# Kernel tuning notes

Hardware: AMD Instinct MI355X
Metric: run time of the kernel (lower is better)

## Reference

```python
import jax, jax.numpy as jnp
import numpy as np

N_NODES = 100000
N_EDGES = 3200000
N_GRAPHS = 64
NEG_SLOPE = 0.2


def mish(x):
    return x * jnp.tanh(jax.nn.softplus(x))


def gat_layer(x, src, dst, W, b, a_src, a_dst, heads, out_ch, n_nodes):
    # h: [N, H, C]
    h = (x @ W).reshape(n_nodes, heads, out_ch)
    alpha_s = jnp.sum(h * a_src[None], axis=-1)  # [N, H]
    alpha_d = jnp.sum(h * a_dst[None], axis=-1)  # [N, H]
    e = jax.nn.leaky_relu(alpha_s[src] + alpha_d[dst], NEG_SLOPE)  # [E, H]
    # scatter-softmax over incoming edges of each destination node
    emax = jax.ops.segment_max(e, dst, num_segments=n_nodes)  # [N, H]
    ee = jnp.exp(e - emax[dst])
    den = jax.ops.segment_sum(ee, dst, num_segments=n_nodes)
    alpha = ee / (den[dst] + 1e-16)  # [E, H]
    msg = h[src] * alpha[..., None]  # [E, H, C]
    out = jax.ops.segment_sum(msg, dst, num_segments=n_nodes)
    return out.reshape(n_nodes, heads * out_ch) + b


def setup_inputs() -> dict:
    key = jax.random.key(0)
    ks = jax.random.split(key, 10)
    x = jax.random.normal(ks[0], (N_NODES, 128), dtype=jnp.float32)
    edge_index = jax.random.randint(ks[1], (2, N_EDGES), 0, N_NODES, dtype=jnp.int64)
    batch = jnp.sort(jax.random.randint(ks[2], (N_NODES,), 0, N_GRAPHS, dtype=jnp.int64))
    s1 = 1.0 / np.sqrt(128.0)
    s2 = 1.0 / np.sqrt(16.0)
    return {
        "x": x,
        "edge_index": edge_index,
        "batch": batch,
        "W1": jax.random.normal(ks[3], (128, 16), dtype=jnp.float32) * s1,
        "b1": jnp.zeros((16,), dtype=jnp.float32),
        "a_src1": jax.random.normal(ks[4], (4, 4), dtype=jnp.float32) * 0.5,
        "a_dst1": jax.random.normal(ks[5], (4, 4), dtype=jnp.float32) * 0.5,
        "W2": jax.random.normal(ks[6], (16, 32), dtype=jnp.float32) * s2,
        "b2": jnp.zeros((32,), dtype=jnp.float32),
        "a_src2": jax.random.normal(ks[7], (1, 32), dtype=jnp.float32) * 0.5,
        "a_dst2": jax.random.normal(ks[8], (1, 32), dtype=jnp.float32) * 0.5,
    }


def reference(x, edge_index, batch, W1, b1, a_src1, a_dst1, W2, b2, a_src2, a_dst2):
    n = x.shape[0]
    # PyG GATConv default add_self_loops=True
    loop = jnp.arange(n, dtype=edge_index.dtype)
    src = jnp.concatenate([edge_index[0], loop])
    dst = jnp.concatenate([edge_index[1], loop])
    h = mish(gat_layer(x, src, dst, W1, b1, a_src1, a_dst1, heads=4, out_ch=4, n_nodes=n))
    h = mish(gat_layer(h, src, dst, W2, b2, a_src2, a_dst2, heads=1, out_ch=32, n_nodes=n))
    # global_mean_pool
    sums = jax.ops.segment_sum(h, batch, num_segments=N_GRAPHS)
    cnts = jax.ops.segment_sum(jnp.ones((n,), h.dtype), batch, num_segments=N_GRAPHS)
    return sums / jnp.maximum(cnts, 1.0)[:, None]
```

## Files before the change

kernel.cpp:

```cpp
#include <hip/hip_runtime.h>
#include <hip/hip_fp16.h>
#include <math.h>

#define NEG_SLOPE 0.2f
#define GB 192
#define SB 320
#define CHMAX 11264
#define CAP 5120
#define CAPH 2560

typedef _Float16 half2v __attribute__((ext_vector_type(2)));
typedef _Float16 half4v __attribute__((ext_vector_type(4)));

__device__ __forceinline__ float mishf(float x) {
    if (x > 15.f) return x;
    float ex = __expf(x);
    float y = 1.f + ex;
    float y2 = y * y;
    return x * (y2 - 1.f) / (y2 + 1.f);
}

__device__ __forceinline__ float lw(float e) {
    return __expf(fmaxf(e, NEG_SLOPE * e));
}

__device__ __forceinline__ float hdot2a(half2v a, half2v b, float c) {
#if __has_builtin(__builtin_amdgcn_fdot2)
    return __builtin_amdgcn_fdot2(a, b, c, false);
#else
    return (float)a.x * (float)b.x + (float)a.y * (float)b.y + c;
#endif
}

__global__ __launch_bounds__(1024) void front_kernel(
        const float* __restrict__ x, const float* __restrict__ W1,
        const float* __restrict__ a_dst,
        const float* __restrict__ W2, const float* __restrict__ as2,
        const float* __restrict__ ad2,
        _Float16* __restrict__ hpre1h, float* __restrict__ addst,
        float* __restrict__ vs, float* __restrict__ vd,
        const int* __restrict__ src, const int* __restrict__ dst,
        int E, int Etot, int CH, int NB, int N, int NT,
        int* __restrict__ cursor, int* __restrict__ pairs) {
    __shared__ __attribute__((aligned(16))) char smem[63824];
    int tid = threadIdx.x;
    if (blockIdx.x < GB) {
        float* Wlt = (float*)smem;
        float* xs  = Wlt + 16 * 132;
        if (blockIdx.x == 0 && tid < 16) {
            float ps = 0.f, pd = 0.f;
            #pragma unroll
            for (int c = 0; c < 32; c++) {
                float w = W2[tid * 32 + c];
                ps += w * as2[c];
                pd += w * ad2[c];
            }
            vs[tid] = ps; vd[tid] = pd;
        }
        for (int i = tid; i < 2048; i += 1024) Wlt[(i & 15) * 132 + (i >> 4)] = W1[i];
        int nl = tid >> 4, ch = tid & 15;
        for (int t = blockIdx.x; t < NT; t += GB) {
            int nodebase = t * 64;
            int nvalid = min(64, N - nodebase);
            __syncthreads();
            const float4* x4 = (const float4*)(x + (size_t)nodebase * 128);
            #pragma unroll
            for (int u = 0; u < 2; u++) {
                int i = tid + (u << 10);
                int tnl = i >> 5;
                if (tnl < nvalid) {
                    float4 v = x4[i];
                    int k = (i & 31) * 4;
                    float* dp = &xs[tnl * 132 + k];
                    dp[0] = v.x; dp[1] = v.y; dp[2] = v.z; dp[3] = v.w;
                }
            }
            __syncthreads();
            if (nl < nvalid) {
                const float4* xr4 = (const float4*)&xs[nl * 132];
                const float4* wr4 = (const float4*)&Wlt[ch * 132];
                float acc = 0.f;
                #pragma unroll
                for (int k4 = 0; k4 < 32; k4++) {
                    float4 xv = xr4[k4];
                    float4 wv = wr4[k4];
                    acc += xv.x * wv.x + xv.y * wv.y + xv.z * wv.z + xv.w * wv.w;
                }
                int node = nodebase + nl;
                hpre1h[node * 16 + ch] = (_Float16)acc;
                float pd = acc * a_dst[ch];
                pd += __shfl_xor(pd, 1); pd += __shfl_xor(pd, 2);
                if ((ch & 3) == 0) addst[node * 4 + (ch >> 2)] = pd;
            }
        }
    } else {
        int nb2 = 2 * NB;
        int* A    = (int*)smem;
        int* Boff = A + nb2;
        int* C    = Boff + nb2;
        int* buf  = C + nb2;
        int blk = blockIdx.x - GB;
        for (int b = tid; b < nb2; b += 1024) A[b] = 0;
        __syncthreads();
        int ibeg = blk * CH, iend = min((blk + 1) * CH, Etot);
        int cdv[11], cs[11];
        #pragma unroll
        for (int u = 0; u < 11; u++) {
            int i = ibeg + tid + (u << 10);
            int d = -1, s = 0;
            if (i < iend) {
                if (i < E) { d = dst[i]; s = src[i]; } else { d = i - E; s = d; }
                atomicAdd(&A[d >> 6], 1);
            }
            cdv[u] = d; cs[u] = s;
        }
        for (int i = ibeg + CHMAX + tid; i < iend; i += 1024) {
            int d, s;
            if (i < E) { d = dst[i]; s = src[i]; } else { d = i - E; s = d; }
            int f = d >> 6;
            int pos = atomicAdd(&cursor[f], 1);
            pos = pos < CAPH ? pos : CAPH - 1;
            size_t addr = (size_t)(f >> 1) * CAP + ((f & 1) ? (CAP - 1 - pos) : pos);
            pairs[addr] = s | ((d & 63) << 17);
        }
        __syncthreads();
        for (int b = tid; b < nb2; b += 1024) Boff[b] = A[b];
        __syncthreads();
        for (int o = 1; o < nb2; o <<= 1) {
            int i1 = tid, i2 = tid + 1024;
            int v1 = 0, v2 = 0;
            if (i1 < nb2 && i1 >= o) v1 = Boff[i1 - o];
            if (i2 < nb2 && i2 >= o) v2 = Boff[i2 - o];
            __syncthreads();
            if (i1 < nb2) Boff[i1] += v1;
            if (i2 < nb2) Boff[i2] += v2;
            __syncthreads();
        }
        for (int b = tid; b < nb2; b += 1024) {
            int cnt = A[b];
            Boff[b] -= cnt;
            C[b] = cnt ? atomicAdd(&cursor[b], cnt) : 0;
        }
        __syncthreads();
        for (int b = tid; b < nb2; b += 1024) A[b] = 0;
        __syncthreads();
        #pragma unroll
        for (int u = 0; u < 11; u++) {
            int d = cdv[u];
            if (d < 0) continue;
            int f = d >> 6;
            int r = atomicAdd(&A[f], 1);
            buf[Boff[f] + r] = cs[u] | ((d & 63) << 17);
        }
        __syncthreads();
        int total = iend - ibeg;
        if (total > CHMAX) total = CHMAX;
        if (total < 0) total = 0;
        for (int j = tid; j < total; j += 1024) {
            int lo = 0, hi = nb2 - 1;
            while (lo < hi) {
                int mid = (lo + hi + 1) >> 1;
                if (Boff[mid] <= j) lo = mid; else hi = mid - 1;
            }
            int f = lo;
            int pos = C[f] + (j - Boff[f]);
            pos = pos < CAPH ? pos : CAPH - 1;
            size_t addr = (size_t)(f >> 1) * CAP + ((f & 1) ? (CAP - 1 - pos) : pos);
            pairs[addr] = buf[j];
        }
    }
}

__global__ __launch_bounds__(256) void csragg1_kernel(
        const int* __restrict__ pairs, const int* __restrict__ btotal,
        int NB, int N,
        int* __restrict__ ssorted, int* __restrict__ rs, int* __restrict__ re,
        const float* __restrict__ a_src1, const float* __restrict__ addst,
        const _Float16* __restrict__ hpre1h, const float* __restrict__ b1,
        const float* __restrict__ vs, const float* __restrict__ vd,
        _Float16* __restrict__ hpost1h,
        float* __restrict__ as2n, float* __restrict__ ad2n) {
    __shared__ int deg[64];
    __shared__ int s[64];
    __shared__ int cur[64];
    __shared__ __attribute__((aligned(16))) int lds_sorted[CAPH];
    int tid = threadIdx.x, bh = blockIdx.x;
    int B = bh >> 1, half = bh & 1;
    int nb0 = (B << 7) + (half << 6);
    int cnt_nodes = min(64, N - nb0);
    int c = min(btotal[bh], CAPH);
    int rbase = B * CAP + (half ? CAP - c : 0);
    if (tid < 64) deg[tid] = 0;
    __syncthreads();
    for (int j = tid; j < c; j += 256)
        atomicAdd(&deg[(pairs[rbase + j] >> 17) & 63], 1);
    __syncthreads();
    if (tid < 64) s[tid] = deg[tid];
    __syncthreads();
    for (int o = 1; o < 64; o <<= 1) {
        int v = 0;
        if (tid < 64 && tid >= o) v = s[tid - o];
        __syncthreads();
        if (tid < 64) s[tid] += v;
        __syncthreads();
    }
    if (tid < 64) {
        int ex = s[tid] - deg[tid];
        cur[tid] = ex;
        if (tid < cnt_nodes) {
            rs[nb0 + tid] = bh * CAPH + ex;
            re[nb0 + tid] = bh * CAPH + ex + deg[tid];
        }
    }
    __syncthreads();
    for (int j = tid; j < c; j += 256) {
        int p = pairs[rbase + j];
        int pos = atomicAdd(&cur[(p >> 17) & 63], 1);
        lds_sorted[pos < CAPH ? pos : CAPH - 1] = p & 0x1FFFF;
    }
    __syncthreads();

    {
        int t4 = c >> 2;
        const int4* ls4 = (const int4*)lds_sorted;
        int4* gs4 = (int4*)(ssorted + (size_t)bh * CAPH);
        for (int j = tid; j < t4; j += 256) gs4[j] = ls4[j];
        for (int j = (t4 << 2) + tid; j < c; j += 256)
            ssorted[(size_t)bh * CAPH + j] = lds_sorted[j];
    }

    int wave = tid >> 6;
    int lane = tid & 63;
    int head = lane & 3, er = lane >> 2;
    int c0 = head * 4;
    half2v w01, w23;
    w01.x = (_Float16)a_src1[c0];     w01.y = (_Float16)a_src1[c0 + 1];
    w23.x = (_Float16)a_src1[c0 + 2]; w23.y = (_Float16)a_src1[c0 + 3];
    for (int r = 0; r < 16; r++) {
        int ln = (wave << 4) + r;
        if (ln >= cnt_nodes) break;
        int node = nb0 + ln;
        int end = cur[ln];
        int start = end - deg[ln];
        float adh = addst[node * 4 + head];
        float den = 0.f, a0 = 0.f, a1 = 0.f, a2 = 0.f, a3 = 0.f;
        int last = end - 1;
        int jb = start;
        for (; jb + 16 <= end; jb += 16) {
            int s0 = lds_sorted[jb + er];
            half4v h = *(const half4v*)(hpre1h + (size_t)s0 * 16 + c0);
            half2v hlo = __builtin_shufflevector(h, h, 0, 1);
            half2v hhi = __builtin_shufflevector(h, h, 2, 3);
            float p = hdot2a(hlo, w01, hdot2a(hhi, w23, 0.f));
            float w = lw(p + adh);
            den += w;
            a0 += (float)h.x * w; a1 += (float)h.y * w;
            a2 += (float)h.z * w; a3 += (float)h.w * w;
        }
        if (jb < end) {
            int j0 = jb + er;
            int k0 = (j0 <= last) ? j0 : last;
            int s0 = lds_sorted[k0];
            half4v h = *(const half4v*)(hpre1h + (size_t)s0 * 16 + c0);
            half2v hlo = __builtin_shufflevector(h, h, 0, 1);
            half2v hhi = __builtin_shufflevector(h, h, 2, 3);
            float p = hdot2a(hlo, w01, hdot2a(hhi, w23, 0.f));
            float w = (j0 <= last) ? lw(p + adh) : 0.f;
            den += w;
            a0 += (float)h.x * w; a1 += (float)h.y * w;
            a2 += (float)h.z * w; a3 += (float)h.w * w;
        }
        a0 += __shfl_xor(a0, 4);  a1 += __shfl_xor(a1, 4);  a2 += __shfl_xor(a2, 4);  a3 += __shfl_xor(a3, 4);  den += __shfl_xor(den, 4);
        a0 += __shfl_xor(a0, 8);  a1 += __shfl_xor(a1, 8);  a2 += __shfl_xor(a2, 8);  a3 += __shfl_xor(a3, 8);  den += __shfl_xor(den, 8);
        a0 += __shfl_xor(a0, 16); a1 += __shfl_xor(a1, 16); a2 += __shfl_xor(a2, 16); a3 += __shfl_xor(a3, 16); den += __shfl_xor(den, 16);
        a0 += __shfl_xor(a0, 32); a1 += __shfl_xor(a1, 32); a2 += __shfl_xor(a2, 32); a3 += __shfl_xor(a3, 32); den += __shfl_xor(den, 32);
        if (er == 0) {
            float inv = 1.f / (den + 1e-16f);
            float o0 = mishf(a0 * inv + b1[c0]);
            float o1 = mishf(a1 * inv + b1[c0 + 1]);
            float o2 = mishf(a2 * inv + b1[c0 + 2]);
            float o3 = mishf(a3 * inv + b1[c0 + 3]);
            half4v oh;
            oh.x = (_Float16)o0; oh.y = (_Float16)o1;
            oh.z = (_Float16)o2; oh.w = (_Float16)o3;
            *(half4v*)(hpost1h + (size_t)node * 16 + c0) = oh;
            float ps = o0 * vs[c0] + o1 * vs[c0 + 1] + o2 * vs[c0 + 2] + o3 * vs[c0 + 3];
            float pd = o0 * vd[c0] + o1 * vd[c0 + 1] + o2 * vd[c0 + 2] + o3 * vd[c0 + 3];
            ps += __shfl_xor(ps, 1); pd += __shfl_xor(pd, 1);
            ps += __shfl_xor(ps, 2); pd += __shfl_xor(pd, 2);
            if (head == 0) { as2n[node] = ps; ad2n[node] = pd; }
        }
    }
}

__global__ void agg2_kernel(const int* __restrict__ rs, const int* __restrict__ re,
                            const int* __restrict__ ssorted,
                            const float* __restrict__ as2n, const float* __restrict__ ad2n,
                            const _Float16* __restrict__ hpost1h,
                            float* __restrict__ agg16, float* __restrict__ denv, int N) {
    int wave = threadIdx.x >> 6;
    int lane = threadIdx.x & 63;
    int node = blockIdx.x * 4 + wave;
    if (node >= N) return;
    int start = rs[node], end = re[node];
    int q = lane & 3, er = lane >> 2;
    int c0 = q * 4;
    float adh = ad2n[node];
    const _Float16* hb = hpost1h + c0;
    float den = 0.f, a0 = 0.f, a1 = 0.f, a2 = 0.f, a3 = 0.f;
    int last = end - 1;
    int jb = start;
    for (; jb + 16 <= end; jb += 16) {
        int s0 = __builtin_nontemporal_load(ssorted + jb + er);
        float w = lw(as2n[s0] + adh);
        half4v h = *(const half4v*)(hb + (size_t)s0 * 16);
        den += w;
        a0 += (float)h.x * w; a1 += (float)h.y * w;
        a2 += (float)h.z * w; a3 += (float)h.w * w;
    }
    if (jb < end) {
        int j0 = jb + er;
        int k0 = (j0 <= last) ? j0 : last;
        int s0 = __builtin_nontemporal_load(ssorted + k0);
        float w = (j0 <= last) ? lw(as2n[s0] + adh) : 0.f;
        half4v h = *(const half4v*)(hb + (size_t)s0 * 16);
        den += w;
        a0 += (float)h.x * w; a1 += (float)h.y * w;
        a2 += (float)h.z * w; a3 += (float)h.w * w;
    }
    a0 += __shfl_xor(a0, 4);  a1 += __shfl_xor(a1, 4);  a2 += __shfl_xor(a2, 4);  a3 += __shfl_xor(a3, 4);  den += __shfl_xor(den, 4);
    a0 += __shfl_xor(a0, 8);  a1 += __shfl_xor(a1, 8);  a2 += __shfl_xor(a2, 8);  a3 += __shfl_xor(a3, 8);  den += __shfl_xor(den, 8);
    a0 += __shfl_xor(a0, 16); a1 += __shfl_xor(a1, 16); a2 += __shfl_xor(a2, 16); a3 += __shfl_xor(a3, 16); den += __shfl_xor(den, 16);
    a0 += __shfl_xor(a0, 32); a1 += __shfl_xor(a1, 32); a2 += __shfl_xor(a2, 32); a3 += __shfl_xor(a3, 32); den += __shfl_xor(den, 32);
    if (er == 0) {
        float4 o; o.x = a0; o.y = a1; o.z = a2; o.w = a3;
        *(float4*)(agg16 + (size_t)node * 16 + c0) = o;
        if (q == 0) denv[node] = den;
    }
}

__global__ void post2pool_kernel(const float* __restrict__ agg16, const float* __restrict__ denv,
                                 const float* __restrict__ W2, const float* __restrict__ b2,
                                 const int* __restrict__ batch,
                                 float* __restrict__ pool, float* __restrict__ cnt, int N) {
    __shared__ float Wl[16 * 32];
    int tid = threadIdx.x;
    for (int i = tid; i < 512; i += 256) Wl[i] = W2[i];
    __syncthreads();
    int r = tid >> 5, ch = tid & 31;
    float bc = b2[ch];
    int base = blockIdx.x * 128;
    int cur = -1;
    float sum = 0.f, c = 0.f;
    for (int it = 0; it < 16; it++) {
        int n = base + it * 8 + r;
        if (n >= N) break;
        int g = batch[n];
        if (g != cur) {
            if (cur >= 0) {
                atomicAdd(&pool[cur * 32 + ch], sum);
                if (ch == 0) atomicAdd(&cnt[cur], c);
            }
            cur = g; sum = 0.f; c = 0.f;
        }
        const float* ar = agg16 + (size_t)n * 16;
        float acc = 0.f;
        #pragma unroll
        for (int k = 0; k < 16; k++) acc += ar[k] * Wl[k * 32 + ch];
        float val = mishf(acc / (denv[n] + 1e-16f) + bc);
        sum += val;
        c += 1.f;
    }
    if (cur >= 0) {
        atomicAdd(&pool[cur * 32 + ch], sum);
        if (ch == 0) atomicAdd(&cnt[cur], c);
    }
}

__global__ void fin_kernel(const float* __restrict__ pool, const float* __restrict__ cnt,
                           float* __restrict__ out, int NG) {
    int i = blockIdx.x * blockDim.x + threadIdx.x;
    if (i >= NG * 32) return;
    out[i] = pool[i] / fmaxf(cnt[i >> 5], 1.0f);
}

extern "C" void kernel_launch(void* const* d_in, const int* in_sizes, int n_in,
                              void* d_out, int out_size, void* d_ws, size_t ws_size,
                              hipStream_t stream) {
    const float* x   = (const float*)d_in[0];
    const int* eidx  = (const int*)d_in[1];
    const int* batch = (const int*)d_in[2];
    const float* W1  = (const float*)d_in[3];
    const float* b1  = (const float*)d_in[4];
    const float* as1 = (const float*)d_in[5];
    const float* ad1 = (const float*)d_in[6];
    const float* W2  = (const float*)d_in[7];
    const float* b2  = (const float*)d_in[8];
    const float* as2 = (const float*)d_in[9];
    const float* ad2 = (const float*)d_in[10];
    float* out = (float*)d_out;

    int N = in_sizes[0] / 128;
    int E = in_sizes[1] / 2;
    int Etot = E + N;
    int NG = out_size / 32;
    const int* esrc = eidx;
    const int* edst = eidx + E;

    int NB = (N + 127) >> 7;
    int NBH = NB * 2;
    int NT = (N + 63) >> 6;
    int CH = (Etot + SB - 1) / SB;

    char* p = (char*)d_ws;
    auto alloc = [&](size_t nbytes) {
        p = (char*)(((uintptr_t)p + 15) & ~(uintptr_t)15);
        void* r = (void*)p; p += nbytes; return r;
    };
    int* pairs        = (int*)alloc((size_t)NB * CAP * 4);
    int* ssorted      = (int*)alloc((size_t)NBH * CAPH * 4);
    int* rs           = (int*)alloc((size_t)N * 4);
    int* re           = (int*)alloc((size_t)N * 4);
    int* cursor       = (int*)alloc((size_t)NBH * 4);
    _Float16* hpre1h  = (_Float16*)alloc((size_t)N * 16 * 2);
    _Float16* hpost1h = (_Float16*)alloc((size_t)N * 16 * 2);
    float* addst1  = (float*)alloc((size_t)N * 4 * 4);
    float* as2n    = (float*)alloc((size_t)N * 4);
    float* ad2n    = (float*)alloc((size_t)N * 4);
    float* agg16   = (float*)alloc((size_t)N * 16 * 4);
    float* denv    = (float*)alloc((size_t)N * 4);
    float* vs      = (float*)alloc(16 * 4);
    float* vd      = (float*)alloc(16 * 4);
    float* pool    = (float*)alloc((size_t)NG * 32 * 4);
    float* cnt     = (float*)alloc((size_t)NG * 4);

    hipMemsetAsync(cursor, 0, (size_t)NBH * 4, stream);
    hipMemsetAsync(pool, 0, (size_t)NG * 32 * 4, stream);
    hipMemsetAsync(cnt, 0, (size_t)NG * 4, stream);

    front_kernel<<<GB + SB, 1024, 0, stream>>>(x, W1, ad1, W2, as2, ad2,
                                               hpre1h, addst1, vs, vd,
                                               esrc, edst, E, Etot, CH, NB, N, NT,
                                               cursor, pairs);
    csragg1_kernel<<<NBH, 256, 0, stream>>>(pairs, cursor, NB, N,
                                            ssorted, rs, re, as1, addst1, hpre1h,
                                            b1, vs, vd, hpost1h, as2n, ad2n);
    agg2_kernel<<<(N + 3) / 4, 256, 0, stream>>>(rs, re, ssorted, as2n, ad2n, hpost1h,
                                                 agg16, denv, N);
    post2pool_kernel<<<(N + 127) / 128, 256, 0, stream>>>(agg16, denv, W2, b2, batch,
                                                          pool, cnt, N);
    fin_kernel<<<(NG * 32 + 255) / 256, 256, 0, stream>>>(pool, cnt, out, NG);
}
```

Measured before the change: 332.9 us.

## Widen per-lane gathers to 16B half8 and double csragg1 block size

The layer-1 and layer-2 aggregation loops now have each lane load 8 halves (16 bytes) per edge instead of 4, with two lanes covering a node's 16 channels. Each lane also handles two edges per iteration, so a wave covers 64 edges at a time and fewer lanes sit in the xor-shuffle reduction. csragg1 moves from 256 to 512 threads per block, so each wave owns 8 nodes instead of 16. This is meant to cut gather instructions and raise memory-level parallelism, at the cost of more wasted lanes on low-degree tails and higher register pressure.

```diff
diff --git a/kernel.cpp b/kernel.cpp
--- a/kernel.cpp
+++ b/kernel.cpp
@@ -11,6 +11,7 @@
 
 typedef _Float16 half2v __attribute__((ext_vector_type(2)));
 typedef _Float16 half4v __attribute__((ext_vector_type(4)));
+typedef _Float16 half8v __attribute__((ext_vector_type(8)));
 
 __device__ __forceinline__ float mishf(float x) {
     if (x > 15.f) return x;
@@ -171,7 +172,7 @@
     }
 }
 
-__global__ __launch_bounds__(256) void csragg1_kernel(
+__global__ __launch_bounds__(512) void csragg1_kernel(
         const int* __restrict__ pairs, const int* __restrict__ btotal,
         int NB, int N,
         int* __restrict__ ssorted, int* __restrict__ rs, int* __restrict__ re,
@@ -192,7 +193,7 @@
     int rbase = B * CAP + (half ? CAP - c : 0);
     if (tid < 64) deg[tid] = 0;
     __syncthreads();
-    for (int j = tid; j < c; j += 256)
+    for (int j = tid; j < c; j += 512)
         atomicAdd(&deg[(pairs[rbase + j] >> 17) & 63], 1);
     __syncthreads();
     if (tid < 64) s[tid] = deg[tid];
@@ -213,7 +214,7 @@
         }
     }
     __syncthreads();
-    for (int j = tid; j < c; j += 256) {
+    for (int j = tid; j < c; j += 512) {
         int p = pairs[rbase + j];
         int pos = atomicAdd(&cur[(p >> 17) & 63], 1);
         lds_sorted[pos < CAPH ? pos : CAPH - 1] = p & 0x1FFFF;
@@ -224,117 +225,170 @@
         int t4 = c >> 2;
         const int4* ls4 = (const int4*)lds_sorted;
         int4* gs4 = (int4*)(ssorted + (size_t)bh * CAPH);
-        for (int j = tid; j < t4; j += 256) gs4[j] = ls4[j];
-        for (int j = (t4 << 2) + tid; j < c; j += 256)
+        for (int j = tid; j < t4; j += 512) gs4[j] = ls4[j];
+        for (int j = (t4 << 2) + tid; j < c; j += 512)
             ssorted[(size_t)bh * CAPH + j] = lds_sorted[j];
     }
 
     int wave = tid >> 6;
     int lane = tid & 63;
-    int head = lane & 3, er = lane >> 2;
-    int c0 = head * 4;
-    half2v w01, w23;
-    w01.x = (_Float16)a_src1[c0];     w01.y = (_Float16)a_src1[c0 + 1];
-    w23.x = (_Float16)a_src1[c0 + 2]; w23.y = (_Float16)a_src1[c0 + 3];
-    for (int r = 0; r < 16; r++) {
-        int ln = (wave << 4) + r;
+    int q = lane & 1, er = lane >> 1;
+    int c0 = q * 8;
+    half2v wA0, wA1, wB0, wB1;
+    wA0.x = (_Float16)a_src1[c0];     wA0.y = (_Float16)a_src1[c0 + 1];
+    wA1.x = (_Float16)a_src1[c0 + 2]; wA1.y = (_Float16)a_src1[c0 + 3];
+    wB0.x = (_Float16)a_src1[c0 + 4]; wB0.y = (_Float16)a_src1[c0 + 5];
+    wB1.x = (_Float16)a_src1[c0 + 6]; wB1.y = (_Float16)a_src1[c0 + 7];
+    for (int r = 0; r < 8; r++) {
+        int ln = (wave << 3) + r;
         if (ln >= cnt_nodes) break;
         int node = nb0 + ln;
         int end = cur[ln];
         int start = end - deg[ln];
-        float adh = addst[node * 4 + head];
-        float den = 0.f, a0 = 0.f, a1 = 0.f, a2 = 0.f, a3 = 0.f;
+        float adh0 = addst[node * 4 + q * 2];
+        float adh1 = addst[node * 4 + q * 2 + 1];
+        float a[8] = {0.f, 0.f, 0.f, 0.f, 0.f, 0.f, 0.f, 0.f};
+        float den0 = 0.f, den1 = 0.f;
         int last = end - 1;
         int jb = start;
-        for (; jb + 16 <= end; jb += 16) {
+        for (; jb + 64 <= end; jb += 64) {
             int s0 = lds_sorted[jb + er];
-            half4v h = *(const half4v*)(hpre1h + (size_t)s0 * 16 + c0);
-            half2v hlo = __builtin_shufflevector(h, h, 0, 1);
-            half2v hhi = __builtin_shufflevector(h, h, 2, 3);
-            float p = hdot2a(hlo, w01, hdot2a(hhi, w23, 0.f));
-            float w = lw(p + adh);
-            den += w;
-            a0 += (float)h.x * w; a1 += (float)h.y * w;
-            a2 += (float)h.z * w; a3 += (float)h.w * w;
+            int s1 = lds_sorted[jb + 32 + er];
+            half8v h0 = *(const half8v*)(hpre1h + (size_t)s0 * 16 + c0);
+            half8v h1 = *(const half8v*)(hpre1h + (size_t)s1 * 16 + c0);
+            half2v h0a = __builtin_shufflevector(h0, h0, 0, 1);
+            half2v h0b = __builtin_shufflevector(h0, h0, 2, 3);
+            half2v h0c = __builtin_shufflevector(h0, h0, 4, 5);
+            half2v h0d = __builtin_shufflevector(h0, h0, 6, 7);
+            half2v h1a = __builtin_shufflevector(h1, h1, 0, 1);
+            half2v h1b = __builtin_shufflevector(h1, h1, 2, 3);
+            half2v h1c = __builtin_shufflevector(h1, h1, 4, 5);
+            half2v h1d = __builtin_shufflevector(h1, h1, 6, 7);
+            float wt00 = lw(hdot2a(h0a, wA0, hdot2a(h0b, wA1, 0.f)) + adh0);
+            float wt01 = lw(hdot2a(h0c, wB0, hdot2a(h0d, wB1, 0.f)) + adh1);
+            float wt10 = lw(hdot2a(h1a, wA0, hdot2a(h1b, wA1, 0.f)) + adh0);
+            float wt11 = lw(hdot2a(h1c, wB0, hdot2a(h1d, wB1, 0.f)) + adh1);
+            den0 += wt00 + wt10; den1 += wt01 + wt11;
+            #pragma unroll
+            for (int k = 0; k < 4; k++) a[k]     += (float)h0[k]     * wt00 + (float)h1[k]     * wt10;
+            #pragma unroll
+            for (int k = 0; k < 4; k++) a[4 + k] += (float)h0[4 + k] * wt01 + (float)h1[4 + k] * wt11;
         }
         if (jb < end) {
-            int j0 = jb + er;
+            int j0 = jb + er, j1 = jb + 32 + er;
             int k0 = (j0 <= last) ? j0 : last;
+            int k1 = (j1 <= last) ? j1 : last;
             int s0 = lds_sorted[k0];
-            half4v h = *(const half4v*)(hpre1h + (size_t)s0 * 16 + c0);
-            half2v hlo = __builtin_shufflevector(h, h, 0, 1);
-            half2v hhi = __builtin_shufflevector(h, h, 2, 3);
-            float p = hdot2a(hlo, w01, hdot2a(hhi, w23, 0.f));
-            float w = (j0 <= last) ? lw(p + adh) : 0.f;
-            den += w;
-            a0 += (float)h.x * w; a1 += (float)h.y * w;
-            a2 += (float)h.z * w; a3 += (float)h.w * w;
-        }
-        a0 += __shfl_xor(a0, 4);  a1 += __shfl_xor(a1, 4);  a2 += __shfl_xor(a2, 4);  a3 += __shfl_xor(a3, 4);  den += __shfl_xor(den, 4);
-        a0 += __shfl_xor(a0, 8);  a1 += __shfl_xor(a1, 8);  a2 += __shfl_xor(a2, 8);  a3 += __shfl_xor(a3, 8);  den += __shfl_xor(den, 8);
-        a0 += __shfl_xor(a0, 16); a1 += __shfl_xor(a1, 16); a2 += __shfl_xor(a2, 16); a3 += __shfl_xor(a3, 16); den += __shfl_xor(den, 16);
-        a0 += __shfl_xor(a0, 32); a1 += __shfl_xor(a1, 32); a2 += __shfl_xor(a2, 32); a3 += __shfl_xor(a3, 32); den += __shfl_xor(den, 32);
+            int s1 = lds_sorted[k1];
+            half8v h0 = *(const half8v*)(hpre1h + (size_t)s0 * 16 + c0);
+            half8v h1 = *(const half8v*)(hpre1h + (size_t)s1 * 16 + c0);
+            half2v h0a = __builtin_shufflevector(h0, h0, 0, 1);
+            half2v h0b = __builtin_shufflevector(h0, h0, 2, 3);
+            half2v h0c = __builtin_shufflevector(h0, h0, 4, 5);
+            half2v h0d = __builtin_shufflevector(h0, h0, 6, 7);
+            half2v h1a = __builtin_shufflevector(h1, h1, 0, 1);
+            half2v h1b = __builtin_shufflevector(h1, h1, 2, 3);
+            half2v h1c = __builtin_shufflevector(h1, h1, 4, 5);
+            half2v h1d = __builtin_shufflevector(h1, h1, 6, 7);
+            float e00 = hdot2a(h0a, wA0, hdot2a(h0b, wA1, 0.f)) + adh0;
+            float e01 = hdot2a(h0c, wB0, hdot2a(h0d, wB1, 0.f)) + adh1;
+            float e10 = hdot2a(h1a, wA0, hdot2a(h1b, wA1, 0.f)) + adh0;
+            float e11 = hdot2a(h1c, wB0, hdot2a(h1d, wB1, 0.f)) + adh1;
+            float wt00 = (j0 <= last) ? lw(e00) : 0.f;
+            float wt01 = (j0 <= last) ? lw(e01) : 0.f;
+            float wt10 = (j1 <= last) ? lw(e10) : 0.f;
+            float wt11 = (j1 <= last) ? lw(e11) : 0.f;
+            den0 += wt00 + wt10; den1 += wt01 + wt11;
+            #pragma unroll
+            for (int k = 0; k < 4; k++) a[k]     += (float)h0[k]     * wt00 + (float)h1[k]     * wt10;
+            #pragma unroll
+            for (int k = 0; k < 4; k++) a[4 + k] += (float)h0[4 + k] * wt01 + (float)h1[4 + k] * wt11;
+        }
+        #pragma unroll
+        for (int off = 2; off <= 32; off <<= 1) {
+            #pragma unroll
+            for (int k = 0; k < 8; k++) a[k] += __shfl_xor(a[k], off);
+            den0 += __shfl_xor(den0, off);
+            den1 += __shfl_xor(den1, off);
+        }
         if (er == 0) {
-            float inv = 1.f / (den + 1e-16f);
-            float o0 = mishf(a0 * inv + b1[c0]);
-            float o1 = mishf(a1 * inv + b1[c0 + 1]);
-            float o2 = mishf(a2 * inv + b1[c0 + 2]);
-            float o3 = mishf(a3 * inv + b1[c0 + 3]);
-            half4v oh;
-            oh.x = (_Float16)o0; oh.y = (_Float16)o1;
-            oh.z = (_Float16)o2; oh.w = (_Float16)o3;
-            *(half4v*)(hpost1h + (size_t)node * 16 + c0) = oh;
-            float ps = o0 * vs[c0] + o1 * vs[c0 + 1] + o2 * vs[c0 + 2] + o3 * vs[c0 + 3];
-            float pd = o0 * vd[c0] + o1 * vd[c0 + 1] + o2 * vd[c0 + 2] + o3 * vd[c0 + 3];
+            float inv0 = 1.f / (den0 + 1e-16f);
+            float inv1 = 1.f / (den1 + 1e-16f);
+            float o[8];
+            #pragma unroll
+            for (int k = 0; k < 4; k++) o[k]     = mishf(a[k]     * inv0 + b1[c0 + k]);
+            #pragma unroll
+            for (int k = 0; k < 4; k++) o[4 + k] = mishf(a[4 + k] * inv1 + b1[c0 + 4 + k]);
+            half8v oh;
+            #pragma unroll
+            for (int k = 0; k < 8; k++) oh[k] = (_Float16)o[k];
+            *(half8v*)(hpost1h + (size_t)node * 16 + c0) = oh;
+            float ps = 0.f, pd = 0.f;
+            #pragma unroll
+            for (int k = 0; k < 8; k++) { ps += o[k] * vs[c0 + k]; pd += o[k] * vd[c0 + k]; }
             ps += __shfl_xor(ps, 1); pd += __shfl_xor(pd, 1);
-            ps += __shfl_xor(ps, 2); pd += __shfl_xor(pd, 2);
-            if (head == 0) { as2n[node] = ps; ad2n[node] = pd; }
-        }
-    }
-}
-
-__global__ void agg2_kernel(const int* __restrict__ rs, const int* __restrict__ re,
-                            const int* __restrict__ ssorted,
-                            const float* __restrict__ as2n, const float* __restrict__ ad2n,
-                            const _Float16* __restrict__ hpost1h,
-                            float* __restrict__ agg16, float* __restrict__ denv, int N) {
+            if (q == 0) { as2n[node] = ps; ad2n[node] = pd; }
+        }
+    }
+}
+
+__global__ __launch_bounds__(256) void agg2_kernel(
+        const int* __restrict__ rs, const int* __restrict__ re,
+        const int* __restrict__ ssorted,
+        const float* __restrict__ as2n, const float* __restrict__ ad2n,
+        const _Float16* __restrict__ hpost1h,
+        float* __restrict__ agg16, float* __restrict__ denv, int N) {
     int wave = threadIdx.x >> 6;
     int lane = threadIdx.x & 63;
     int node = blockIdx.x * 4 + wave;
     if (node >= N) return;
     int start = rs[node], end = re[node];
-    int q = lane & 3, er = lane >> 2;
-    int c0 = q * 4;
+    int q = lane & 1, er = lane >> 1;
+    int c0 = q * 8;
     float adh = ad2n[node];
     const _Float16* hb = hpost1h + c0;
-    float den = 0.f, a0 = 0.f, a1 = 0.f, a2 = 0.f, a3 = 0.f;
+    float a[8] = {0.f, 0.f, 0.f, 0.f, 0.f, 0.f, 0.f, 0.f};
+    float den = 0.f;
     int last = end - 1;
     int jb = start;
-    for (; jb + 16 <= end; jb += 16) {
+    for (; jb + 64 <= end; jb += 64) {
         int s0 = __builtin_nontemporal_load(ssorted + jb + er);
-        float w = lw(as2n[s0] + adh);
-        half4v h = *(const half4v*)(hb + (size_t)s0 * 16);
-        den += w;
-        a0 += (float)h.x * w; a1 += (float)h.y * w;
-        a2 += (float)h.z * w; a3 += (float)h.w * w;
+        int s1 = __builtin_nontemporal_load(ssorted + jb + 32 + er);
+        float wt0 = lw(as2n[s0] + adh);
+        float wt1 = lw(as2n[s1] + adh);
+        half8v h0 = *(const half8v*)(hb + (size_t)s0 * 16);
+        half8v h1 = *(const half8v*)(hb + (size_t)s1 * 16);
+        den += wt0 + wt1;
+        #pragma unroll
+        for (int k = 0; k < 8; k++) a[k] += (float)h0[k] * wt0 + (float)h1[k] * wt1;
     }
     if (jb < end) {
-        int j0 = jb + er;
+        int j0 = jb + er, j1 = jb + 32 + er;
         int k0 = (j0 <= last) ? j0 : last;
+        int k1 = (j1 <= last) ? j1 : last;
         int s0 = __builtin_nontemporal_load(ssorted + k0);
-        float w = (j0 <= last) ? lw(as2n[s0] + adh) : 0.f;
-        half4v h = *(const half4v*)(hb + (size_t)s0 * 16);
-        den += w;
-        a0 += (float)h.x * w; a1 += (float)h.y * w;
-        a2 += (float)h.z * w; a3 += (float)h.w * w;
-    }
-    a0 += __shfl_xor(a0, 4);  a1 += __shfl_xor(a1, 4);  a2 += __shfl_xor(a2, 4);  a3 += __shfl_xor(a3, 4);  den += __shfl_xor(den, 4);
-    a0 += __shfl_xor(a0, 8);  a1 += __shfl_xor(a1, 8);  a2 += __shfl_xor(a2, 8);  a3 += __shfl_xor(a3, 8);  den += __shfl_xor(den, 8);
-    a0 += __shfl_xor(a0, 16); a1 += __shfl_xor(a1, 16); a2 += __shfl_xor(a2, 16); a3 += __shfl_xor(a3, 16); den += __shfl_xor(den, 16);
-    a0 += __shfl_xor(a0, 32); a1 += __shfl_xor(a1, 32); a2 += __shfl_xor(a2, 32); a3 += __shfl_xor(a3, 32); den += __shfl_xor(den, 32);
+        int s1 = __builtin_nontemporal_load(ssorted + k1);
+        float wt0 = (j0 <= last) ? lw(as2n[s0] + adh) : 0.f;
+        float wt1 = (j1 <= last) ? lw(as2n[s1] + adh) : 0.f;
+        half8v h0 = *(const half8v*)(hb + (size_t)s0 * 16);
+        half8v h1 = *(const half8v*)(hb + (size_t)s1 * 16);
+        den += wt0 + wt1;
+        #pragma unroll
+        for (int k = 0; k < 8; k++) a[k] += (float)h0[k] * wt0 + (float)h1[k] * wt1;
+    }
+    #pragma unroll
+    for (int off = 2; off <= 32; off <<= 1) {
+        #pragma unroll
+        for (int k = 0; k < 8; k++) a[k] += __shfl_xor(a[k], off);
+        den += __shfl_xor(den, off);
+    }
     if (er == 0) {
-        float4 o; o.x = a0; o.y = a1; o.z = a2; o.w = a3;
-        *(float4*)(agg16 + (size_t)node * 16 + c0) = o;
+        float4 o0, o1;
+        o0.x = a[0]; o0.y = a[1]; o0.z = a[2]; o0.w = a[3];
+        o1.x = a[4]; o1.y = a[5]; o1.z = a[6]; o1.w = a[7];
+        float* ag = agg16 + (size_t)node * 16 + c0;
+        *(float4*)ag = o0;
+        *(float4*)(ag + 4) = o1;
         if (q == 0) denv[node] = den;
     }
 }
@@ -442,7 +496,7 @@
                                                hpre1h, addst1, vs, vd,
                                                esrc, edst, E, Etot, CH, NB, N, NT,
                                                cursor, pairs);
-    csragg1_kernel<<<NBH, 256, 0, stream>>>(pairs, cursor, NB, N,
+    csragg1_kernel<<<NBH, 512, 0, stream>>>(pairs, cursor, NB, N,
                                             ssorted, rs, re, as1, addst1, hpre1h,
                                             b1, vs, vd, hpost1h, as2n, ad2n);
     agg2_kernel<<<(N + 3) / 4, 256, 0, stream>>>(rs, re, ssorted, as2n, ad2n, hpost1h,
```

Measured after the change: 361.4 us. 1.09x slower.
